# Performance work log

Hardware: AMD Instinct MI355X
Metric: run time of the kernel (lower is better)

## Reference

```python
import jax, jax.numpy as jnp
import numpy as np

B, F, O = 32, 26, 20
IN, G = 2048, 512
REL = 53
EPS = 1e-5  # BatchNorm1d default eps


def setup_inputs() -> dict:
    key = jax.random.key(0)
    ks = jax.random.split(key, 10)
    inp = {
        "region_feats": jax.random.normal(ks[0], (B, F, O, IN), jnp.float32),
        "region_masks": jnp.ones((B, F, O), jnp.float32),
        "rel_feats": jax.random.randint(ks[1], (B, F, O, O), 0, REL, jnp.int64),
        "tem_feats": jax.random.uniform(ks[2], (B, F * O, F * O), jnp.float32),
        # learned params (eval mode: dropout off, BN uses running stats)
        "rel_W": jax.random.normal(ks[3], (G, IN), jnp.float32) * (1.0 / np.sqrt(IN)),
        "rel_b": jnp.zeros((G,), jnp.float32),
        "rel_emb": jax.random.normal(ks[4], (REL, G), jnp.float32) * 0.02,
        "tem_W": jax.random.normal(ks[5], (G, IN), jnp.float32) * (1.0 / np.sqrt(IN)),
        "tem_b": jnp.zeros((G,), jnp.float32),
        "bn_w": jnp.ones((F * O,), jnp.float32),
        "bn_b": jnp.zeros((F * O,), jnp.float32),
        "bn_rm": jnp.zeros((F * O,), jnp.float32),
        "bn_rv": jnp.ones((F * O,), jnp.float32),
    }
    return inp


def reference(region_feats, region_masks, rel_feats, tem_feats,
              rel_W, rel_b, rel_emb, tem_W, tem_b,
              bn_w, bn_b, bn_rm, bn_rv):
    b, f, o, _ = region_feats.shape
    # ---- RELATIONAL FEATURE GRAPH ----
    # [B,F,O,G]
    rel_region = jnp.einsum("bfoi,gi->bfog", region_feats, rel_W) + rel_b
    # embedding lookup: [B,F,O,O,G]
    emb = rel_emb[rel_feats]
    mask = (rel_feats > 0).astype(region_feats.dtype)  # [B,F,O,O]
    msum = jnp.sum(mask, axis=3)                        # [B,F,O]
    # sum_j mask_ij * emb_ij  (masked reduction over neighbor dim)
    emb_sum = jnp.einsum("bfijg,bfij->bfig", emb, mask)
    # sum_j mask_ij * r_i == r_i * msum_i, so (emb_sum + r*msum)/msum
    rel_out = (emb_sum + rel_region * msum[..., None]) / msum[..., None]
    rel_out = rel_out.reshape(b, f * o, -1)
    # ---- TEMPORAL FEATURE GRAPH ----
    tem_region = jnp.einsum("bfoi,gi->bfog", region_feats, tem_W) + tem_b
    tem_region = tem_region.reshape(b, f * o, -1)
    tem_sum = jnp.sum(tem_feats, axis=2)                # [B, F*O]
    tem_out = jnp.matmul(tem_feats, tem_region) / tem_sum[..., None]
    # ---- OUTPUT ----
    out = jnp.concatenate([rel_out, tem_out], axis=-1)  # [B, F*O, 2G]
    out = jnp.tanh(out)
    # BatchNorm1d over channel dim 1 (eval mode, running stats)
    inv = bn_w / jnp.sqrt(bn_rv + EPS)                  # [F*O]
    out = (out - bn_rm[None, :, None]) * inv[None, :, None] + bn_b[None, :, None]
    return out
```

## Files before the change

kernel.cpp:

```cpp
#include <hip/hip_runtime.h>
#include <stdint.h>

#define BB 32
#define FO 520
#define M1 16640
#define KIN 2048
#define KA 2112
#define N1 1024
#define GG 512
#define K2P 576
#define M2 640

typedef unsigned short u16;
typedef short v8s __attribute__((ext_vector_type(8)));
typedef float v4f __attribute__((ext_vector_type(4)));

__device__ __forceinline__ u16 f2bf(float f) {
  union { float f; unsigned u; } v; v.f = f;
  unsigned r = v.u + 0x7fffu + ((v.u >> 16) & 1u);
  return (u16)(r >> 16);
}

__device__ __forceinline__ float fast_tanh(float x) {
  float cx = fminf(fmaxf(x, -15.f), 15.f);
  float e = __expf(2.f * cx);
  return (e - 1.f) / (e + 1.f);
}

#define PREP_ROWS 8832
__global__ __launch_bounds__(512) void prep_all_kernel(
    const float* __restrict__ rf, const int* __restrict__ rel,
    const float* __restrict__ relW, const float* __restrict__ temW,
    const float* __restrict__ emb, const float* __restrict__ tem,
    u16* __restrict__ A1, u16* __restrict__ Wc,
    u16* __restrict__ A2, float* __restrict__ tsum) {
  const int blk = blockIdx.x;
  const int t = threadIdx.x;
  if (blk < PREP_ROWS) {
    const int row = blk * 2 + (t >> 8);
    const int tt = t & 255;
    const float* src;
    u16* orow;
    if (row < M1) { src = rf + (size_t)row * KIN; orow = A1 + (size_t)row * KA; }
    else {
      const int n = row - M1;
      src = (n < GG) ? (relW + (size_t)n * KIN) : (temW + (size_t)(n - GG) * KIN);
      orow = Wc + (size_t)n * KA;
    }
    const v4f* p = (const v4f*)src;
    v4f a = __builtin_nontemporal_load(p + 2 * tt);
    v4f b = __builtin_nontemporal_load(p + 2 * tt + 1);
    v8s v;
    v[0] = (short)f2bf(a[0]); v[1] = (short)f2bf(a[1]);
    v[2] = (short)f2bf(a[2]); v[3] = (short)f2bf(a[3]);
    v[4] = (short)f2bf(b[0]); v[5] = (short)f2bf(b[1]);
    v[6] = (short)f2bf(b[2]); v[7] = (short)f2bf(b[3]);
    *(v8s*)(orow + tt * 8) = v;
    if (tt < 64) {
      float sval = 0.f;
      if (row < M1) {
        const int* rp = rel + (size_t)row * 20;
        int cnt = 0, ms = 0;
#pragma unroll
        for (int j = 0; j < 20; ++j) { int ix = rp[j]; cnt += (ix == tt + 1); ms += (ix > 0); }
        if (tt < 52 && ms > 0) sval = (float)cnt / (float)ms;
      } else {
        const int n = row - M1;
        if (n < GG && tt < 52) sval = emb[(size_t)(tt + 1) * GG + n];
      }
      orow[KIN + tt] = f2bf(sval);
    }
    return;
  }
  const int w = t >> 6, l = t & 63;
  const int row = (blk - PREP_ROWS) * 8 + w;
  const int b = row / M2, i = row % M2;
  u16* orow = A2 + (size_t)row * K2P;
  v8s z = {0, 0, 0, 0, 0, 0, 0, 0};
  if (i >= FO) {
    *(v8s*)(orow + l * 8) = z;
    if (l < 8) *(v8s*)(orow + (64 + l) * 8) = z;
    return;
  }
  const float* srow = tem + ((size_t)b * FO + i) * FO;
  float s = 0.f;
  {
    v4f a = __builtin_nontemporal_load((const v4f*)(srow + 8 * l));
    v4f bb = __builtin_nontemporal_load((const v4f*)(srow + 8 * l + 4));
    s += a[0] + a[1] + a[2] + a[3] + bb[0] + bb[1] + bb[2] + bb[3];
    v8s v;
    v[0] = (short)f2bf(a[0]); v[1] = (short)f2bf(a[1]);
    v[2] = (short)f2bf(a[2]); v[3] = (short)f2bf(a[3]);
    v[4] = (short)f2bf(bb[0]); v[5] = (short)f2bf(bb[1]);
    v[6] = (short)f2bf(bb[2]); v[7] = (short)f2bf(bb[3]);
    *(v8s*)(orow + l * 8) = v;
  }
  if (l < 8) {
    if (l == 0) {
      v4f a = __builtin_nontemporal_load((const v4f*)(srow + 512));
      v4f bb = __builtin_nontemporal_load((const v4f*)(srow + 516));
      s += a[0] + a[1] + a[2] + a[3] + bb[0] + bb[1] + bb[2] + bb[3];
      v8s v;
      v[0] = (short)f2bf(a[0]); v[1] = (short)f2bf(a[1]);
      v[2] = (short)f2bf(a[2]); v[3] = (short)f2bf(a[3]);
      v[4] = (short)f2bf(bb[0]); v[5] = (short)f2bf(bb[1]);
      v[6] = (short)f2bf(bb[2]); v[7] = (short)f2bf(bb[3]);
      *(v8s*)(orow + 512) = v;
    } else {
      *(v8s*)(orow + (64 + l) * 8) = z;
    }
  }
#pragma unroll
  for (int off = 32; off > 0; off >>= 1) s += __shfl_down(s, off);
  if (l == 0) tsum[(size_t)b * FO + i] = s;
}

#define G1_STAGE(DST)                                                                            \
  do {                                                                                           \
    u16* dst_ = smem + (DST);                                                                    \
    __builtin_amdgcn_global_load_lds((const __attribute__((address_space(1))) void*)ga0,         \
        (__attribute__((address_space(3))) void*)(dst_ + lofA0), 16, 0, 0);                      \
    __builtin_amdgcn_global_load_lds((const __attribute__((address_space(1))) void*)ga1,         \
        (__attribute__((address_space(3))) void*)(dst_ + lofA1), 16, 0, 0);                      \
    __builtin_amdgcn_global_load_lds((const __attribute__((address_space(1))) void*)gb0,         \
        (__attribute__((address_space(3))) void*)(dst_ + lofB0), 16, 0, 0);                      \
    ga0 += 32; ga1 += 32; gb0 += 32;                                                             \
  } while (0)

#define G1_COMPUTE(CB)                                                                           \
  do {                                                                                           \
    const u16* As_ = smem + (CB) * 12288;                                                        \
    const u16* Bs_ = As_ + 8192;                                                                 \
    v8s af[4], bf[4];                                                                            \
    _Pragma("unroll") for (int t4 = 0; t4 < 4; ++t4) {                                           \
      const int ra = wm * 64 + t4 * 16 + r16;                                                    \
      const int rb = wn * 64 + t4 * 16 + r16;                                                    \
      af[t4] = *(const v8s*)&As_[ra * 32 + ((quad ^ ((ra >> 1) & 3)) * 8)];                      \
      bf[t4] = *(const v8s*)&Bs_[rb * 32 + ((quad ^ ((rb >> 1) & 3)) * 8)];                      \
    }                                                                                            \
    _Pragma("unroll") for (int mtt = 0; mtt < 4; ++mtt)                                          \
      _Pragma("unroll") for (int ntt = 0; ntt < 4; ++ntt)                                        \
        acc[mtt][ntt] =                                                                          \
            __builtin_amdgcn_mfma_f32_16x16x32_bf16(af[mtt], bf[ntt], acc[mtt][ntt], 0, 0, 0);   \
  } while (0)

__global__ __launch_bounds__(512, 4) void gemm1_kernel(
    const u16* __restrict__ A, const u16* __restrict__ Wc,
    const float* __restrict__ rel_b, const float* __restrict__ tem_b,
    const float* __restrict__ bn_w, const float* __restrict__ bn_b,
    const float* __restrict__ bn_rm, const float* __restrict__ bn_rv,
    float* __restrict__ out, u16* __restrict__ BT) {
  __shared__ u16 smem[36864];
  const int tid = threadIdx.x;
  const int lane = tid & 63;
  const int wv = tid >> 6, wm = wv >> 1, wn = wv & 1;
  const int id = blockIdx.x;
  const int wgid = (id & 7) * 65 + (id >> 3);
  const int mt = wgid >> 3, nt = wgid & 7;
  const int m0 = mt * 256, n0 = nt * 128;
  const int quad = lane >> 4, r16 = lane & 15;

  const u16 *ga0, *ga1, *gb0;
  {
    const int r0 = tid >> 2, sl0 = tid & 3;
    ga0 = A + (size_t)(m0 + r0) * KA + (sl0 ^ ((r0 >> 1) & 3)) * 8;
    const int r1 = 128 + (tid >> 2);
    ga1 = A + (size_t)(m0 + r1) * KA + (sl0 ^ ((r1 >> 1) & 3)) * 8;
    gb0 = Wc + (size_t)(n0 + r0) * KA + (sl0 ^ ((r0 >> 1) & 3)) * 8;
  }
  const int lofA0 = wv * 512;
  const int lofA1 = 4096 + wv * 512;
  const int lofB0 = 8192 + wv * 512;

  v4f acc[4][4];
#pragma unroll
  for (int i = 0; i < 4; ++i)
#pragma unroll
    for (int j = 0; j < 4; ++j) { v4f z = {0.f, 0.f, 0.f, 0.f}; acc[i][j] = z; }

  G1_STAGE(0);
  G1_STAGE(12288);

  int cb = 0, nb = 2;
  for (int t = 0; t < 64; ++t) {
    G1_STAGE(nb * 12288);
    asm volatile("s_waitcnt vmcnt(6)" ::: "memory");
    __builtin_amdgcn_s_barrier();
    G1_COMPUTE(cb);
    asm volatile("s_waitcnt lgkmcnt(0)" ::: "memory");
    __builtin_amdgcn_s_barrier();
    cb = (cb == 2) ? 0 : cb + 1;
    nb = (nb == 2) ? 0 : nb + 1;
  }
  {
    const int cb1 = (cb == 2) ? 0 : cb + 1;
    asm volatile("s_waitcnt vmcnt(3)" ::: "memory");
    __builtin_amdgcn_s_barrier();
    G1_COMPUTE(cb);
    asm volatile("s_waitcnt vmcnt(0) lgkmcnt(0)" ::: "memory");
    __builtin_amdgcn_s_barrier();
    G1_COMPUTE(cb1);
  }

  if (n0 < GG) {
#pragma unroll
    for (int mtt = 0; mtt < 4; ++mtt) {
      const int mb = m0 + wm * 64 + mtt * 16 + quad * 4;
      const int bb = mb / FO;
      const int fo0 = mb - bb * FO;
      float inv[4], rm[4], bofs[4];
#pragma unroll
      for (int r = 0; r < 4; ++r) {
        const int fo = fo0 + r;
        inv[r] = bn_w[fo] * rsqrtf(bn_rv[fo] + 1e-5f);
        rm[r] = bn_rm[fo]; bofs[r] = bn_b[fo];
      }
#pragma unroll
      for (int ntt = 0; ntt < 4; ++ntt) {
        const int n = n0 + wn * 64 + ntt * 16 + r16;
        const float rbn = rel_b[n];
#pragma unroll
        for (int r = 0; r < 4; ++r) {
          float val = (fast_tanh(acc[mtt][ntt][r] + rbn) - rm[r]) * inv[r] + bofs[r];
          __builtin_nontemporal_store(val, out + (size_t)(mb + r) * N1 + n);
        }
      }
    }
  } else {
    __syncthreads();
#pragma unroll
    for (int p = 0; p < 2; ++p) {
      if (p) __syncthreads();
      if (wn == p) {
#pragma unroll
        for (int mtt = 0; mtt < 4; ++mtt) {
          const int il = wm * 64 + mtt * 16 + quad * 4;
#pragma unroll
          for (int ntt = 0; ntt < 4; ++ntt) {
            const int gl = ntt * 16 + r16;
            const float tb = tem_b[(n0 - GG) + p * 64 + gl];
            ushort4 w;
            w.x = f2bf(acc[mtt][ntt][0] + tb);
            w.y = f2bf(acc[mtt][ntt][1] + tb);
            w.z = f2bf(acc[mtt][ntt][2] + tb);
            w.w = f2bf(acc[mtt][ntt][3] + tb);
            *(ushort4*)&smem[gl * 264 + il] = w;
          }
        }
      }
      __syncthreads();
#pragma unroll
      for (int pass = 0; pass < 4; ++pass) {
        const int gl = pass * 16 + (tid >> 5);
        const int ch = tid & 31;
        const int m = m0 + ch * 8;
        const int b1 = m / FO;
        const int i1 = m - b1 * FO;
        v8s val = *(const v8s*)&smem[gl * 264 + ch * 8];
        const int g = (n0 - GG) + p * 64 + gl;
        *(v8s*)(BT + ((size_t)(b1 * GG + g)) * K2P + i1) = val;
      }
    }
  }
}

#define G2_STAGE(DST)                                                                            \
  do {                                                                                           \
    u16* dst_ = smem + (DST);                                                                    \
    __builtin_amdgcn_global_load_lds((const __attribute__((address_space(1))) void*)ga0,         \
        (__attribute__((address_space(3))) void*)(dst_ + lofA0), 16, 0, 0);                      \
    __builtin_amdgcn_global_load_lds((const __attribute__((address_space(1))) void*)gb0,         \
        (__attribute__((address_space(3))) void*)(dst_ + lofB0), 16, 0, 0);                      \
    __builtin_amdgcn_global_load_lds((const __attribute__((address_space(1))) void*)gb1,         \
        (__attribute__((address_space(3))) void*)(dst_ + lofB1), 16, 0, 0);                      \
    ga0 += 32; gb0 += 32; gb1 += 32;                                                             \
  } while (0)

#define G2_COMPUTE(CB)                                                                           \
  do {                                                                                           \
    const u16* As_ = smem + (CB) * 12288;                                                        \
    const u16* Bs_ = As_ + 4096;                                                                 \
    v8s af[4], bf[4];                                                                            \
    _Pragma("unroll") for (int t4 = 0; t4 < 4; ++t4) {                                           \
      const int ra = wm * 64 + t4 * 16 + r16;                                                    \
      const int rb = wn * 64 + t4 * 16 + r16;                                                    \
      af[t4] = *(const v8s*)&As_[ra * 32 + ((quad ^ ((ra >> 1) & 3)) * 8)];                      \
      bf[t4] = *(const v8s*)&Bs_[rb * 32 + ((quad ^ ((rb >> 1) & 3)) * 8)];                      \
    }                                                                                            \
    _Pragma("unroll") for (int mtt = 0; mtt < 4; ++mtt)                                          \
      _Pragma("unroll") for (int ntt = 0; ntt < 4; ++ntt)                                        \
        acc[mtt][ntt] =                                                                          \
            __builtin_amdgcn_mfma_f32_16x16x32_bf16(af[mtt], bf[ntt], acc[mtt][ntt], 0, 0, 0);   \
  } while (0)

__global__ __launch_bounds__(512, 4) void gemm2_kernel(
    const u16* __restrict__ A2, const u16* __restrict__ BT,
    const float* __restrict__ tsum,
    const float* __restrict__ bn_w, const float* __restrict__ bn_b,
    const float* __restrict__ bn_rm, const float* __restrict__ bn_rv,
    float* __restrict__ out) {
  __shared__ u16 smem[36864];
  const int tid = threadIdx.x;
  const int lane = tid & 63;
  const int wv = tid >> 6, wm = wv >> 2, wn = wv & 3;
  const int m0 = blockIdx.x * 128;
  const int n0 = blockIdx.y * 256;
  const int b = blockIdx.z;
  const u16* Ab = A2 + (size_t)b * M2 * K2P;
  const u16* Bb = BT + (size_t)b * GG * K2P;
  const int quad = lane >> 4, r16 = lane & 15;

  const u16 *ga0, *gb0, *gb1;
  {
    const int r0 = tid >> 2, sl0 = tid & 3;
    const int c0 = (sl0 ^ ((r0 >> 1) & 3)) * 8;
    ga0 = Ab + (size_t)(m0 + r0) * K2P + c0;
    gb0 = Bb + (size_t)(n0 + r0) * K2P + c0;
    gb1 = Bb + (size_t)(n0 + 128 + r0) * K2P + c0;
  }
  const int lofA0 = wv * 512;
  const int lofB0 = 4096 + wv * 512;
  const int lofB1 = 8192 + wv * 512;

  v4f acc[4][4];
#pragma unroll
  for (int i = 0; i < 4; ++i)
#pragma unroll
    for (int j = 0; j < 4; ++j) { v4f z = {0.f, 0.f, 0.f, 0.f}; acc[i][j] = z; }

  G2_STAGE(0);
  G2_STAGE(12288);

  int cb = 0, nb = 2;
  for (int t = 0; t < 16; ++t) {
    G2_STAGE(nb * 12288);
    asm volatile("s_waitcnt vmcnt(6)" ::: "memory");
    __builtin_amdgcn_s_barrier();
    G2_COMPUTE(cb);
    asm volatile("s_waitcnt lgkmcnt(0)" ::: "memory");
    __builtin_amdgcn_s_barrier();
    cb = (cb == 2) ? 0 : cb + 1;
    nb = (nb == 2) ? 0 : nb + 1;
  }
  {
    const int cb1 = (cb == 2) ? 0 : cb + 1;
    asm volatile("s_waitcnt vmcnt(3)" ::: "memory");
    __builtin_amdgcn_s_barrier();
    G2_COMPUTE(cb);
    asm volatile("s_waitcnt vmcnt(0) lgkmcnt(0)" ::: "memory");
    __builtin_amdgcn_s_barrier();
    G2_COMPUTE(cb1);
  }

#pragma unroll
  for (int mtt = 0; mtt < 4; ++mtt) {
    const int ibase = m0 + wm * 64 + mtt * 16 + quad * 4;
    if (ibase >= FO) continue;
    float ts[4], inv[4], rm[4], bofs[4];
#pragma unroll
    for (int r = 0; r < 4; ++r) {
      const int i = ibase + r;
      ts[r] = 1.f / tsum[(size_t)b * FO + i];
      inv[r] = bn_w[i] * rsqrtf(bn_rv[i] + 1e-5f);
      rm[r] = bn_rm[i]; bofs[r] = bn_b[i];
    }
#pragma unroll
    for (int ntt = 0; ntt < 4; ++ntt) {
      const int g = n0 + wn * 64 + ntt * 16 + r16;
#pragma unroll
      for (int r = 0; r < 4; ++r) {
        float val = (fast_tanh(acc[mtt][ntt][r] * ts[r]) - rm[r]) * inv[r] + bofs[r];
        __builtin_nontemporal_store(val, out + ((size_t)(b * FO + (ibase + r))) * N1 + GG + g);
      }
    }
  }
}

extern "C" void kernel_launch(void* const* d_in, const int* in_sizes, int n_in,
                              void* d_out, int out_size, void* d_ws, size_t ws_size,
                              hipStream_t stream) {
  const float* region_feats = (const float*)d_in[0];
  const int* rel_feats = (const int*)d_in[2];
  const float* tem_feats = (const float*)d_in[3];
  const float* rel_W = (const float*)d_in[4];
  const float* rel_b = (const float*)d_in[5];
  const float* rel_emb = (const float*)d_in[6];
  const float* tem_W = (const float*)d_in[7];
  const float* tem_b = (const float*)d_in[8];
  const float* bn_w = (const float*)d_in[9];
  const float* bn_b = (const float*)d_in[10];
  const float* bn_rm = (const float*)d_in[11];
  const float* bn_rv = (const float*)d_in[12];
  float* out = (float*)d_out;

  char* base = (char*)d_ws;
  u16* A1 = (u16*)base;
  u16* Wc = (u16*)(base + 70287360);
  u16* A2 = (u16*)(base + 74612736);
  u16* BT = (u16*)(base + 98205696);
  float* tsum = (float*)(base + 117080064);

  prep_all_kernel<<<PREP_ROWS + 2560, 512, 0, stream>>>(
      region_feats, rel_feats, rel_W, tem_W, rel_emb, tem_feats, A1, Wc, A2, tsum);
  gemm1_kernel<<<520, 512, 0, stream>>>(A1, Wc, rel_b, tem_b,
                                        bn_w, bn_b, bn_rm, bn_rv, out, BT);
  gemm2_kernel<<<dim3(5, 2, 32), 512, 0, stream>>>(A2, BT, tsum,
                                                   bn_w, bn_b, bn_rm, bn_rv, out);
}
```

Before: 389.4 us.

## Use 4-wave gemm1 blocks with 128x64 per-wave tiles

Halves the gemm1 workgroup from 8 waves to 4 while keeping the 256x128 block tile, so each wave now computes a 128x64 sub-tile with an 8x4 MFMA accumulator array. Each thread issues six async global-to-LDS loads per stage instead of three, and the vmcnt waits and epilogue loops are adjusted to match. The aim is more MFMA work per LDS fragment read and less barrier overhead per block. The cost is roughly double the accumulator registers per wave, which lowers occupancy and may cause spills.

```diff
diff --git a/kernel.cpp b/kernel.cpp
--- a/kernel.cpp
+++ b/kernel.cpp
@@ -25,6 +25,11 @@
   float cx = fminf(fmaxf(x, -15.f), 15.f);
   float e = __expf(2.f * cx);
   return (e - 1.f) / (e + 1.f);
+}
+
+__device__ __forceinline__ void glds(const u16* g, u16* l) {
+  __builtin_amdgcn_global_load_lds((const __attribute__((address_space(1))) void*)g,
+                                   (__attribute__((address_space(3))) void*)l, 16, 0, 0);
 }
 
 #define PREP_ROWS 8832
@@ -117,34 +122,33 @@
 
 #define G1_STAGE(DST)                                                                            \
   do {                                                                                           \
-    u16* dst_ = smem + (DST);                                                                    \
-    __builtin_amdgcn_global_load_lds((const __attribute__((address_space(1))) void*)ga0,         \
-        (__attribute__((address_space(3))) void*)(dst_ + lofA0), 16, 0, 0);                      \
-    __builtin_amdgcn_global_load_lds((const __attribute__((address_space(1))) void*)ga1,         \
-        (__attribute__((address_space(3))) void*)(dst_ + lofA1), 16, 0, 0);                      \
-    __builtin_amdgcn_global_load_lds((const __attribute__((address_space(1))) void*)gb0,         \
-        (__attribute__((address_space(3))) void*)(dst_ + lofB0), 16, 0, 0);                      \
-    ga0 += 32; ga1 += 32; gb0 += 32;                                                             \
+    u16* dst_ = smem + (DST) + tid * 8;                                                          \
+    glds(ga0, dst_);         glds(ga1, dst_ + 2048);                                             \
+    glds(ga2, dst_ + 4096);  glds(ga3, dst_ + 6144);                                             \
+    glds(gb0, dst_ + 8192);  glds(gb1, dst_ + 10240);                                            \
+    ga0 += 32; ga1 += 32; ga2 += 32; ga3 += 32; gb0 += 32; gb1 += 32;                            \
   } while (0)
 
 #define G1_COMPUTE(CB)                                                                           \
   do {                                                                                           \
     const u16* As_ = smem + (CB) * 12288;                                                        \
     const u16* Bs_ = As_ + 8192;                                                                 \
-    v8s af[4], bf[4];                                                                            \
-    _Pragma("unroll") for (int t4 = 0; t4 < 4; ++t4) {                                           \
-      const int ra = wm * 64 + t4 * 16 + r16;                                                    \
-      const int rb = wn * 64 + t4 * 16 + r16;                                                    \
-      af[t4] = *(const v8s*)&As_[ra * 32 + ((quad ^ ((ra >> 1) & 3)) * 8)];                      \
-      bf[t4] = *(const v8s*)&Bs_[rb * 32 + ((quad ^ ((rb >> 1) & 3)) * 8)];                      \
+    v8s af[8], bf[4];                                                                            \
+    _Pragma("unroll") for (int i = 0; i < 8; ++i) {                                              \
+      const int ra = wm * 128 + i * 16 + r16;                                                    \
+      af[i] = *(const v8s*)&As_[ra * 32 + ((quad ^ ((ra >> 1) & 3)) * 8)];                       \
     }                                                                                            \
-    _Pragma("unroll") for (int mtt = 0; mtt < 4; ++mtt)                                          \
-      _Pragma("unroll") for (int ntt = 0; ntt < 4; ++ntt)                                        \
-        acc[mtt][ntt] =                                                                          \
-            __builtin_amdgcn_mfma_f32_16x16x32_bf16(af[mtt], bf[ntt], acc[mtt][ntt], 0, 0, 0);   \
+    _Pragma("unroll") for (int j = 0; j < 4; ++j) {                                              \
+      const int rb = wn * 64 + j * 16 + r16;                                                     \
+      bf[j] = *(const v8s*)&Bs_[rb * 32 + ((quad ^ ((rb >> 1) & 3)) * 8)];                       \
+    }                                                                                            \
+    _Pragma("unroll") for (int i = 0; i < 8; ++i)                                                \
+      _Pragma("unroll") for (int j = 0; j < 4; ++j)                                              \
+        acc[i][j] =                                                                              \
+            __builtin_amdgcn_mfma_f32_16x16x32_bf16(af[i], bf[j], acc[i][j], 0, 0, 0);           \
   } while (0)
 
-__global__ __launch_bounds__(512, 4) void gemm1_kernel(
+__global__ __launch_bounds__(256, 2) void gemm1_kernel(
     const u16* __restrict__ A, const u16* __restrict__ Wc,
     const float* __restrict__ rel_b, const float* __restrict__ tem_b,
     const float* __restrict__ bn_w, const float* __restrict__ bn_b,
@@ -160,21 +164,21 @@
   const int m0 = mt * 256, n0 = nt * 128;
   const int quad = lane >> 4, r16 = lane & 15;
 
-  const u16 *ga0, *ga1, *gb0;
+  const u16 *ga0, *ga1, *ga2, *ga3, *gb0, *gb1;
   {
     const int r0 = tid >> 2, sl0 = tid & 3;
-    ga0 = A + (size_t)(m0 + r0) * KA + (sl0 ^ ((r0 >> 1) & 3)) * 8;
-    const int r1 = 128 + (tid >> 2);
-    ga1 = A + (size_t)(m0 + r1) * KA + (sl0 ^ ((r1 >> 1) & 3)) * 8;
-    gb0 = Wc + (size_t)(n0 + r0) * KA + (sl0 ^ ((r0 >> 1) & 3)) * 8;
-  }
-  const int lofA0 = wv * 512;
-  const int lofA1 = 4096 + wv * 512;
-  const int lofB0 = 8192 + wv * 512;
-
-  v4f acc[4][4];
-#pragma unroll
-  for (int i = 0; i < 4; ++i)
+    const int c0 = (sl0 ^ ((r0 >> 1) & 3)) * 8;
+    ga0 = A + (size_t)(m0 + r0) * KA + c0;
+    ga1 = A + (size_t)(m0 + 64 + r0) * KA + c0;
+    ga2 = A + (size_t)(m0 + 128 + r0) * KA + c0;
+    ga3 = A + (size_t)(m0 + 192 + r0) * KA + c0;
+    gb0 = Wc + (size_t)(n0 + r0) * KA + c0;
+    gb1 = Wc + (size_t)(n0 + 64 + r0) * KA + c0;
+  }
+
+  v4f acc[8][4];
+#pragma unroll
+  for (int i = 0; i < 8; ++i)
 #pragma unroll
     for (int j = 0; j < 4; ++j) { v4f z = {0.f, 0.f, 0.f, 0.f}; acc[i][j] = z; }
 
@@ -184,7 +188,7 @@
   int cb = 0, nb = 2;
   for (int t = 0; t < 64; ++t) {
     G1_STAGE(nb * 12288);
-    asm volatile("s_waitcnt vmcnt(6)" ::: "memory");
+    asm volatile("s_waitcnt vmcnt(12)" ::: "memory");
     __builtin_amdgcn_s_barrier();
     G1_COMPUTE(cb);
     asm volatile("s_waitcnt lgkmcnt(0)" ::: "memory");
@@ -194,7 +198,7 @@
   }
   {
     const int cb1 = (cb == 2) ? 0 : cb + 1;
-    asm volatile("s_waitcnt vmcnt(3)" ::: "memory");
+    asm volatile("s_waitcnt vmcnt(6)" ::: "memory");
     __builtin_amdgcn_s_barrier();
     G1_COMPUTE(cb);
     asm volatile("s_waitcnt vmcnt(0) lgkmcnt(0)" ::: "memory");
@@ -204,8 +208,8 @@
 
   if (n0 < GG) {
 #pragma unroll
-    for (int mtt = 0; mtt < 4; ++mtt) {
-      const int mb = m0 + wm * 64 + mtt * 16 + quad * 4;
+    for (int mtt = 0; mtt < 8; ++mtt) {
+      const int mb = m0 + wm * 128 + mtt * 16 + quad * 4;
       const int bb = mb / FO;
       const int fo0 = mb - bb * FO;
       float inv[4], rm[4], bofs[4];
@@ -233,8 +237,8 @@
       if (p) __syncthreads();
       if (wn == p) {
 #pragma unroll
-        for (int mtt = 0; mtt < 4; ++mtt) {
-          const int il = wm * 64 + mtt * 16 + quad * 4;
+        for (int mtt = 0; mtt < 8; ++mtt) {
+          const int il = wm * 128 + mtt * 16 + quad * 4;
 #pragma unroll
           for (int ntt = 0; ntt < 4; ++ntt) {
             const int gl = ntt * 16 + r16;
@@ -250,8 +254,8 @@
       }
       __syncthreads();
 #pragma unroll
-      for (int pass = 0; pass < 4; ++pass) {
-        const int gl = pass * 16 + (tid >> 5);
+      for (int pass = 0; pass < 8; ++pass) {
+        const int gl = pass * 8 + (tid >> 5);
         const int ch = tid & 31;
         const int m = m0 + ch * 8;
         const int b1 = m / FO;
@@ -267,12 +271,7 @@
 #define G2_STAGE(DST)                                                                            \
   do {                                                                                           \
     u16* dst_ = smem + (DST);                                                                    \
-    __builtin_amdgcn_global_load_lds((const __attribute__((address_space(1))) void*)ga0,         \
-        (__attribute__((address_space(3))) void*)(dst_ + lofA0), 16, 0, 0);                      \
-    __builtin_amdgcn_global_load_lds((const __attribute__((address_space(1))) void*)gb0,         \
-        (__attribute__((address_space(3))) void*)(dst_ + lofB0), 16, 0, 0);                      \
-    __builtin_amdgcn_global_load_lds((const __attribute__((address_space(1))) void*)gb1,         \
-        (__attribute__((address_space(3))) void*)(dst_ + lofB1), 16, 0, 0);                      \
+    glds(ga0, dst_ + lofA0); glds(gb0, dst_ + lofB0); glds(gb1, dst_ + lofB1);                   \
     ga0 += 32; gb0 += 32; gb1 += 32;                                                             \
   } while (0)
 
@@ -402,7 +401,7 @@
 
   prep_all_kernel<<<PREP_ROWS + 2560, 512, 0, stream>>>(
       region_feats, rel_feats, rel_W, tem_W, rel_emb, tem_feats, A1, Wc, A2, tsum);
-  gemm1_kernel<<<520, 512, 0, stream>>>(A1, Wc, rel_b, tem_b,
+  gemm1_kernel<<<520, 256, 0, stream>>>(A1, Wc, rel_b, tem_b,
                                         bn_w, bn_b, bn_rm, bn_rv, out, BT);
   gemm2_kernel<<<dim3(5, 2, 32), 512, 0, stream>>>(A2, BT, tsum,
                                                    bn_w, bn_b, bn_rm, bn_rv, out);
```

Result: slower. 398.3 us (+2.3%).
